# Performance work log

Measured on AMD Instinct MI355X. Metric: run time of the kernel, lower is better.

## Reference

```python
import jax, jax.numpy as jnp
import numpy as np

B, T, I = 16384, 50, 5
H = 128
PRED_LEN = 12


def _uniform(key, shape, bound):
    return jax.random.uniform(key, shape, jnp.float32, -bound, bound)


def setup_inputs() -> dict:
    key = jax.random.key(0)
    ks = jax.random.split(key, 12)
    bound = 1.0 / np.sqrt(H)  # PyTorch LSTM/Linear default init
    return {
        "x": jax.random.normal(ks[0], (B, T, I), jnp.float32),
        "enc_Wih": _uniform(ks[1], (4 * H, I), bound),
        "enc_Whh": _uniform(ks[2], (4 * H, H), bound),
        "enc_bih": _uniform(ks[3], (4 * H,), bound),
        "enc_bhh": _uniform(ks[4], (4 * H,), bound),
        "dec_Wih": _uniform(ks[5], (4 * H, I), bound),
        "dec_Whh": _uniform(ks[6], (4 * H, H), bound),
        "dec_bih": _uniform(ks[7], (4 * H,), bound),
        "dec_bhh": _uniform(ks[8], (4 * H,), bound),
        "lin_W": _uniform(ks[9], (2, H), bound),
        "lin_b": _uniform(ks[10], (2,), bound),
    }


def _lstm_cell(x_t, h, c, Wih, Whh, bih, bhh):
    # PyTorch gate order: i, f, g, o
    gates = x_t @ Wih.T + h @ Whh.T + (bih + bhh)  # [B, 4H]
    i, f, g, o = jnp.split(gates, 4, axis=-1)
    i = jax.nn.sigmoid(i)
    f = jax.nn.sigmoid(f)
    g = jnp.tanh(g)
    o = jax.nn.sigmoid(o)
    c_new = f * c + i * g
    h_new = o * jnp.tanh(c_new)
    return h_new, c_new


def reference(x, enc_Wih, enc_Whh, enc_bih, enc_bhh,
              dec_Wih, dec_Whh, dec_bih, dec_bhh, lin_W, lin_b):
    b = x.shape[0]
    h0 = jnp.zeros((b, H), x.dtype)
    c0 = jnp.zeros((b, H), x.dtype)

    # ---- encoder LSTM over the history sequence ----
    def enc_step(carry, x_t):
        h, c = carry
        h, c = _lstm_cell(x_t, h, c, enc_Wih, enc_Whh, enc_bih, enc_bhh)
        return (h, c), None

    (h, c), _ = jax.lax.scan(enc_step, (h0, c0), jnp.swapaxes(x, 0, 1))

    static_context = x[:, -1, 2:]          # [B, I-2]
    last_velocity = x[:, -1, :2]           # [B, 2]
    dec_in0 = jnp.concatenate([last_velocity, static_context], axis=1)  # [B, I]

    def dec_step(carry, _):
        h, c, dec_in = carry
        h, c = _lstm_cell(dec_in, h, c, dec_Wih, dec_Whh, dec_bih, dec_bhh)
        pred = h @ lin_W.T + lin_b                      # [B, 2]
        dec_in = jnp.concatenate([pred, static_context], axis=1)
        return (h, c, dec_in), pred

    _, preds = jax.lax.scan(dec_step, (h, c, dec_in0), None, length=PRED_LEN)
    return jnp.swapaxes(preds, 0, 1)  # [B, pred_len, 2]
```

## Files before the change

### kernel.cpp

```cpp
#include <hip/hip_runtime.h>
#include <cstdint>

#define TT 50
#define II 5
#define PRED 12

typedef _Float16 f16;
typedef _Float16 f16x8 __attribute__((ext_vector_type(8)));
typedef float f32x4 __attribute__((ext_vector_type(4)));

__global__ void prep_weights(const float* __restrict__ Wih, const float* __restrict__ Whh,
                             const float* __restrict__ bih, const float* __restrict__ bhh,
                             f16* __restrict__ outw) {
    int f = blockIdx.x * 256 + threadIdx.x;
    if (f >= 81920) return;
    int j  = f & 7;
    int c  = (f >> 3) & 15;
    int q  = (f >> 7) & 3;
    int t2 = f >> 9;
    int kc = t2 % 5;
    int wg = t2 / 5;
    int w = wg >> 2, gsub = wg & 3;
    int g = gsub * 128 + w * 16 + c;
    int k = kc * 32 + q * 8 + j;
    float v;
    if (k < 128)       v = Whh[g * 128 + k];
    else if (k < 133)  v = Wih[g * 5 + (k - 128)];
    else if (k == 133) v = bih[g] + bhh[g];
    else               v = 0.f;
    outw[f] = (f16)v;
}

__device__ __forceinline__ float fsig(float x) {
    return __builtin_amdgcn_rcpf(1.f + __builtin_amdgcn_exp2f(-1.4426950408889634f * x));
}
__device__ __forceinline__ float ftanh(float x) {
    return 1.f - 2.f * __builtin_amdgcn_rcpf(1.f + __builtin_amdgcn_exp2f(2.885390081777927f * x));
}

__global__ __launch_bounds__(512, 2)
void lstm_kernel(const float* __restrict__ x,
                 const f16* __restrict__ wfrag,
                 const float* __restrict__ linW, const float* __restrict__ linB,
                 float* __restrict__ out) {
    __shared__ __align__(16) unsigned char state[64 * 512];
    __shared__ float predpart[8][64][2];

    const int tid  = threadIdx.x;
    const int lane = tid & 63;
    const int w    = tid >> 6;
    const int q    = lane >> 4;
    const int cl   = lane & 15;
    const int s0   = blockIdx.x * 64;
    const int jb   = w * 16 + q * 4;
    const int physh = ((jb >> 3) ^ (2 * cl)) & 31;
    const int hoff  = (jb & 7) * 2;

    f16x8 wr[4][5];
    {
        const f16x8* wp = (const f16x8*)wfrag;
        #pragma unroll
        for (int gs = 0; gs < 4; ++gs) {
            #pragma unroll
            for (int kc = 0; kc < 5; ++kc)
                wr[gs][kc] = wp[((w * 4 + gs) * 5 + kc) * 64 + lane];
        }
    }
    float w0r[4], w1r[4];
    #pragma unroll
    for (int idx = 0; idx < 4; ++idx) {
        w0r[idx] = linW[jb + idx];
        w1r[idx] = linW[128 + jb + idx];
    }
    float sc0 = 0.f, sc1 = 0.f, sc2 = 0.f;
    if (tid < 64) {
        const float* xr = x + (size_t)(s0 + tid) * (TT * II) + 49 * II;
        sc0 = xr[2]; sc1 = xr[3]; sc2 = xr[4];
    }
    {
        uint32_t* sp = (uint32_t*)state;
        #pragma unroll
        for (int r = 0; r < 16; ++r) sp[tid + r * 512] = 0u;
    }
    float creg[4][4];
    #pragma unroll
    for (int a = 0; a < 4; ++a)
        #pragma unroll
        for (int b = 0; b < 4; ++b) creg[a][b] = 0.f;

    __syncthreads();
    if (tid < 64) {
        const float* xr = x + (size_t)(s0 + tid) * (TT * II);
        union { f16 h[8]; uint4 u; } pk;
        pk.h[0] = (f16)xr[0]; pk.h[1] = (f16)xr[1]; pk.h[2] = (f16)xr[2];
        pk.h[3] = (f16)xr[3]; pk.h[4] = (f16)xr[4];
        pk.h[5] = (f16)1.f; pk.h[6] = (f16)0.f; pk.h[7] = (f16)0.f;
        int phys = 16 ^ (2 * (tid & 15));
        *(uint4*)(state + tid * 512 + phys * 16) = pk.u;
    }
    __syncthreads();

    f32x4 zero4 = {0.f, 0.f, 0.f, 0.f};

    #pragma unroll 1
    for (int t = 0; t < TT; ++t) {
        float xv0 = 0, xv1 = 0, xv2 = 0, xv3 = 0, xv4 = 0;
        if (tid < 64) {
            int tn = (t < TT - 1) ? t + 1 : TT - 1;
            const float* xr = x + (size_t)(s0 + tid) * (TT * II) + tn * II;
            xv0 = xr[0]; xv1 = xr[1]; xv2 = xr[2]; xv3 = xr[3]; xv4 = xr[4];
        }
        f32x4 acc[4][4];
        #pragma unroll
        for (int gs = 0; gs < 4; ++gs)
            #pragma unroll
            for (int ns = 0; ns < 4; ++ns) acc[gs][ns] = zero4;

        #pragma unroll
        for (int ns = 0; ns < 4; ++ns) {
            const int srow = ns * 16 + cl;
            #pragma unroll
            for (int kc = 0; kc < 5; ++kc) {
                const int phys = (kc * 4 + q) ^ (2 * cl);
                f16x8 bf = *(const f16x8*)(state + srow * 512 + phys * 16);
                acc[0][ns] = __builtin_amdgcn_mfma_f32_16x16x32_f16(wr[0][kc], bf, acc[0][ns], 0, 0, 0);
                acc[1][ns] = __builtin_amdgcn_mfma_f32_16x16x32_f16(wr[1][kc], bf, acc[1][ns], 0, 0, 0);
                acc[2][ns] = __builtin_amdgcn_mfma_f32_16x16x32_f16(wr[2][kc], bf, acc[2][ns], 0, 0, 0);
                acc[3][ns] = __builtin_amdgcn_mfma_f32_16x16x32_f16(wr[3][kc], bf, acc[3][ns], 0, 0, 0);
            }
        }
        uint2 hp[4];
        #pragma unroll
        for (int ns = 0; ns < 4; ++ns) {
            union { f16 h[4]; uint2 u; } pk;
            #pragma unroll
            for (int idx = 0; idx < 4; ++idx) {
                float ii = fsig(acc[0][ns][idx]);
                float ff = fsig(acc[1][ns][idx]);
                float gg = ftanh(acc[2][ns][idx]);
                float oo = fsig(acc[3][ns][idx]);
                float cn = ff * creg[ns][idx] + ii * gg;
                creg[ns][idx] = cn;
                pk.h[idx] = (f16)(oo * ftanh(cn));
            }
            hp[ns] = pk.u;
        }
        __syncthreads();
        #pragma unroll
        for (int ns = 0; ns < 4; ++ns)
            *(uint2*)(state + (ns * 16 + cl) * 512 + physh * 16 + hoff) = hp[ns];
        if (tid < 64) {
            union { f16 h[8]; uint4 u; } pk;
            pk.h[0] = (f16)xv0; pk.h[1] = (f16)xv1; pk.h[2] = (f16)xv2;
            pk.h[3] = (f16)xv3; pk.h[4] = (f16)xv4;
            pk.h[5] = (f16)1.f; pk.h[6] = (f16)0.f; pk.h[7] = (f16)0.f;
            int phys = 16 ^ (2 * (tid & 15));
            *(uint4*)(state + tid * 512 + phys * 16) = pk.u;
        }
        __syncthreads();
    }

    {
        const f16x8* wp = (const f16x8*)(wfrag + 81920);
        #pragma unroll
        for (int gs = 0; gs < 4; ++gs) {
            #pragma unroll
            for (int kc = 0; kc < 5; ++kc)
                wr[gs][kc] = wp[((w * 4 + gs) * 5 + kc) * 64 + lane];
        }
    }

    #pragma unroll 1
    for (int td = 0; td < PRED; ++td) {
        f32x4 acc[4][4];
        #pragma unroll
        for (int gs = 0; gs < 4; ++gs)
            #pragma unroll
            for (int ns = 0; ns < 4; ++ns) acc[gs][ns] = zero4;

        #pragma unroll
        for (int ns = 0; ns < 4; ++ns) {
            const int srow = ns * 16 + cl;
            #pragma unroll
            for (int kc = 0; kc < 5; ++kc) {
                const int phys = (kc * 4 + q) ^ (2 * cl);
                f16x8 bf = *(const f16x8*)(state + srow * 512 + phys * 16);
                acc[0][ns] = __builtin_amdgcn_mfma_f32_16x16x32_f16(wr[0][kc], bf, acc[0][ns], 0, 0, 0);
                acc[1][ns] = __builtin_amdgcn_mfma_f32_16x16x32_f16(wr[1][kc], bf, acc[1][ns], 0, 0, 0);
                acc[2][ns] = __builtin_amdgcn_mfma_f32_16x16x32_f16(wr[2][kc], bf, acc[2][ns], 0, 0, 0);
                acc[3][ns] = __builtin_amdgcn_mfma_f32_16x16x32_f16(wr[3][kc], bf, acc[3][ns], 0, 0, 0);
            }
        }
        uint2 hp[4];
        float p0[4], p1[4];
        #pragma unroll
        for (int ns = 0; ns < 4; ++ns) {
            union { f16 h[4]; uint2 u; } pk;
            p0[ns] = 0.f; p1[ns] = 0.f;
            #pragma unroll
            for (int idx = 0; idx < 4; ++idx) {
                float ii = fsig(acc[0][ns][idx]);
                float ff = fsig(acc[1][ns][idx]);
                float gg = ftanh(acc[2][ns][idx]);
                float oo = fsig(acc[3][ns][idx]);
                float cn = ff * creg[ns][idx] + ii * gg;
                creg[ns][idx] = cn;
                float hv = oo * ftanh(cn);
                p0[ns] += hv * w0r[idx];
                p1[ns] += hv * w1r[idx];
                pk.h[idx] = (f16)hv;
            }
            hp[ns] = pk.u;
        }
        #pragma unroll
        for (int ns = 0; ns < 4; ++ns) {
            p0[ns] += __shfl_xor(p0[ns], 16);
            p0[ns] += __shfl_xor(p0[ns], 32);
            p1[ns] += __shfl_xor(p1[ns], 16);
            p1[ns] += __shfl_xor(p1[ns], 32);
        }
        if (q == 0) {
            #pragma unroll
            for (int ns = 0; ns < 4; ++ns) {
                predpart[w][ns * 16 + cl][0] = p0[ns];
                predpart[w][ns * 16 + cl][1] = p1[ns];
            }
        }
        __syncthreads();
        #pragma unroll
        for (int ns = 0; ns < 4; ++ns)
            *(uint2*)(state + (ns * 16 + cl) * 512 + physh * 16 + hoff) = hp[ns];
        if (tid < 64) {
            float a0 = linB[0], a1 = linB[1];
            #pragma unroll
            for (int ww = 0; ww < 8; ++ww) {
                a0 += predpart[ww][tid][0];
                a1 += predpart[ww][tid][1];
            }
            float2 o2; o2.x = a0; o2.y = a1;
            *(float2*)(out + (size_t)(s0 + tid) * (PRED * 2) + td * 2) = o2;
            union { f16 h[8]; uint4 u; } pk;
            pk.h[0] = (f16)a0; pk.h[1] = (f16)a1;
            pk.h[2] = (f16)sc0; pk.h[3] = (f16)sc1; pk.h[4] = (f16)sc2;
            pk.h[5] = (f16)1.f; pk.h[6] = (f16)0.f; pk.h[7] = (f16)0.f;
            int phys = 16 ^ (2 * (tid & 15));
            *(uint4*)(state + tid * 512 + phys * 16) = pk.u;
        }
        __syncthreads();
    }
}

extern "C" void kernel_launch(void* const* d_in, const int* in_sizes, int n_in,
                              void* d_out, int out_size, void* d_ws, size_t ws_size,
                              hipStream_t stream) {
    (void)in_sizes; (void)n_in; (void)out_size; (void)ws_size;
    const float* x    = (const float*)d_in[0];
    const float* eWih = (const float*)d_in[1];
    const float* eWhh = (const float*)d_in[2];
    const float* ebih = (const float*)d_in[3];
    const float* ebhh = (const float*)d_in[4];
    const float* dWih = (const float*)d_in[5];
    const float* dWhh = (const float*)d_in[6];
    const float* dbih = (const float*)d_in[7];
    const float* dbhh = (const float*)d_in[8];
    const float* linW = (const float*)d_in[9];
    const float* linB = (const float*)d_in[10];
    f16* wfrag = (f16*)d_ws;

    prep_weights<<<320, 256, 0, stream>>>(eWih, eWhh, ebih, ebhh, wfrag);
    prep_weights<<<320, 256, 0, stream>>>(dWih, dWhh, dbih, dbhh, wfrag + 81920);
    lstm_kernel<<<256, 512, 0, stream>>>(x, wfrag, linW, linB, (float*)d_out);
}
```

Before: 281.0 us.

## Split batch tile into two half-groups and overlap MFMA with activations

The 64-sample tile is split into two 32-sample halves (A and B) with double-buffered LDS state. In the encoder, the MFMA for one half is interleaved with the gate activations of the other, so matrix and transcendental work can overlap within each barrier interval. The weight-prep kernels are removed and weights are converted to fp16 fragments directly in registers inside the main kernel. The cell activation is rewritten with fewer reciprocals and a clamped tanh. This adds LDS usage and register pressure, and every block now converts the weights itself, repeating that work across all blocks.

```diff
diff --git a/kernel.cpp b/kernel.cpp
--- a/kernel.cpp
+++ b/kernel.cpp
@@ -9,42 +9,123 @@
 typedef _Float16 f16x8 __attribute__((ext_vector_type(8)));
 typedef float f32x4 __attribute__((ext_vector_type(4)));
 
-__global__ void prep_weights(const float* __restrict__ Wih, const float* __restrict__ Whh,
-                             const float* __restrict__ bih, const float* __restrict__ bhh,
-                             f16* __restrict__ outw) {
-    int f = blockIdx.x * 256 + threadIdx.x;
-    if (f >= 81920) return;
-    int j  = f & 7;
-    int c  = (f >> 3) & 15;
-    int q  = (f >> 7) & 3;
-    int t2 = f >> 9;
-    int kc = t2 % 5;
-    int wg = t2 / 5;
-    int w = wg >> 2, gsub = wg & 3;
-    int g = gsub * 128 + w * 16 + c;
-    int k = kc * 32 + q * 8 + j;
-    float v;
-    if (k < 128)       v = Whh[g * 128 + k];
-    else if (k < 133)  v = Wih[g * 5 + (k - 128)];
-    else if (k == 133) v = bih[g] + bhh[g];
-    else               v = 0.f;
-    outw[f] = (f16)v;
-}
-
-__device__ __forceinline__ float fsig(float x) {
-    return __builtin_amdgcn_rcpf(1.f + __builtin_amdgcn_exp2f(-1.4426950408889634f * x));
-}
-__device__ __forceinline__ float ftanh(float x) {
-    return 1.f - 2.f * __builtin_amdgcn_rcpf(1.f + __builtin_amdgcn_exp2f(2.885390081777927f * x));
+#define K1 1.4426950408889634f
+#define K2 2.8853900817779268f
+
+__device__ __forceinline__ float cellact(float xi, float xf, float xg, float xo, float& c) {
+    float ea = __builtin_amdgcn_exp2f(xi * -K1);
+    float ef = __builtin_amdgcn_exp2f(xf * -K1);
+    float eg = __builtin_amdgcn_exp2f(xg *  K2);
+    float eo = __builtin_amdgcn_exp2f(xo * -K1);
+    float a1 = 1.f + ea, a2 = 1.f + ef, a3 = eg + 1.f, a4 = eg - 1.f;
+    float t1 = a1 * a3;
+    float cn = fmaf(c, t1, a4 * a2) * __builtin_amdgcn_rcpf(t1 * a2);
+    c = cn;
+    float cc = fminf(fmaxf(cn, -15.f), 15.f);
+    float ec = __builtin_amdgcn_exp2f(cc * K2);
+    return (ec - 1.f) * __builtin_amdgcn_rcpf((1.f + eo) * (ec + 1.f));
+}
+
+__device__ __forceinline__ void load_weights(const float* __restrict__ Wih, const float* __restrict__ Whh,
+                                             const float* __restrict__ bih, const float* __restrict__ bhh,
+                                             f16x8 wr[4][5], int w, int cl, int q) {
+    #pragma unroll
+    for (int gs = 0; gs < 4; ++gs) {
+        const int g = gs * 128 + w * 16 + cl;
+        const float* row = Whh + g * 128 + q * 8;
+        #pragma unroll
+        for (int kc = 0; kc < 4; ++kc) {
+            float4 a = *(const float4*)(row + kc * 32);
+            float4 b = *(const float4*)(row + kc * 32 + 4);
+            f16x8 r;
+            r[0] = (f16)a.x; r[1] = (f16)a.y; r[2] = (f16)a.z; r[3] = (f16)a.w;
+            r[4] = (f16)b.x; r[5] = (f16)b.y; r[6] = (f16)b.z; r[7] = (f16)b.w;
+            wr[gs][kc] = r;
+        }
+        f16x8 r;
+        #pragma unroll
+        for (int j = 0; j < 8; ++j) {
+            int k = 128 + q * 8 + j;
+            float v = 0.f;
+            if (k < 133)       v = Wih[g * 5 + (k - 128)];
+            else if (k == 133) v = bih[g] + bhh[g];
+            r[j] = (f16)v;
+        }
+        wr[gs][4] = r;
+    }
+}
+
+__device__ __forceinline__ void do_mfma(const unsigned char* sb, const f16x8 wr[4][5],
+                                        f32x4 acc[4][2], int cl, int q) {
+    #pragma unroll
+    for (int ns = 0; ns < 2; ++ns) {
+        const int srow = ns * 16 + cl;
+        #pragma unroll
+        for (int kc = 0; kc < 5; ++kc) {
+            const int phys = (kc * 4 + q) ^ (2 * cl);
+            f16x8 bf = *(const f16x8*)(sb + srow * 512 + phys * 16);
+            acc[0][ns] = __builtin_amdgcn_mfma_f32_16x16x32_f16(wr[0][kc], bf, acc[0][ns], 0, 0, 0);
+            acc[1][ns] = __builtin_amdgcn_mfma_f32_16x16x32_f16(wr[1][kc], bf, acc[1][ns], 0, 0, 0);
+            acc[2][ns] = __builtin_amdgcn_mfma_f32_16x16x32_f16(wr[2][kc], bf, acc[2][ns], 0, 0, 0);
+            acc[3][ns] = __builtin_amdgcn_mfma_f32_16x16x32_f16(wr[3][kc], bf, acc[3][ns], 0, 0, 0);
+        }
+    }
+}
+
+__device__ __forceinline__ void do_act(f32x4 acc[4][2], float creg[2][4], unsigned char* dst,
+                                       int cl, int physh, int hoff) {
+    #pragma unroll
+    for (int ns = 0; ns < 2; ++ns) {
+        union { f16 h[4]; uint2 u; } pk;
+        #pragma unroll
+        for (int idx = 0; idx < 4; ++idx)
+            pk.h[idx] = (f16)cellact(acc[0][ns][idx], acc[1][ns][idx], acc[2][ns][idx],
+                                     acc[3][ns][idx], creg[ns][idx]);
+        *(uint2*)(dst + (ns * 16 + cl) * 512 + physh * 16 + hoff) = pk.u;
+    }
+}
+
+__device__ __forceinline__ void do_act_dec(f32x4 acc[4][2], float creg[2][4], unsigned char* dst,
+                                           int cl, int physh, int hoff,
+                                           const float w0r[4], const float w1r[4],
+                                           float p0[2], float p1[2]) {
+    #pragma unroll
+    for (int ns = 0; ns < 2; ++ns) {
+        union { f16 h[4]; uint2 u; } pk;
+        p0[ns] = 0.f; p1[ns] = 0.f;
+        #pragma unroll
+        for (int idx = 0; idx < 4; ++idx) {
+            float hv = cellact(acc[0][ns][idx], acc[1][ns][idx], acc[2][ns][idx],
+                               acc[3][ns][idx], creg[ns][idx]);
+            p0[ns] = fmaf(hv, w0r[idx], p0[ns]);
+            p1[ns] = fmaf(hv, w1r[idx], p1[ns]);
+            pk.h[idx] = (f16)hv;
+        }
+        *(uint2*)(dst + (ns * 16 + cl) * 512 + physh * 16 + hoff) = pk.u;
+    }
+}
+
+__device__ __forceinline__ void write_x5(unsigned char* sb, int sl,
+                                         float v0, float v1, float v2, float v3, float v4) {
+    union { f16 h[8]; uint4 u; } pk;
+    pk.h[0] = (f16)v0; pk.h[1] = (f16)v1; pk.h[2] = (f16)v2;
+    pk.h[3] = (f16)v3; pk.h[4] = (f16)v4;
+    pk.h[5] = (f16)1.f; pk.h[6] = (f16)0.f; pk.h[7] = (f16)0.f;
+    int phys = 16 ^ (2 * (sl & 15));
+    *(uint4*)(sb + sl * 512 + phys * 16) = pk.u;
 }
 
 __global__ __launch_bounds__(512, 2)
 void lstm_kernel(const float* __restrict__ x,
-                 const f16* __restrict__ wfrag,
+                 const float* __restrict__ eWih, const float* __restrict__ eWhh,
+                 const float* __restrict__ ebih, const float* __restrict__ ebhh,
+                 const float* __restrict__ dWih, const float* __restrict__ dWhh,
+                 const float* __restrict__ dbih, const float* __restrict__ dbhh,
                  const float* __restrict__ linW, const float* __restrict__ linB,
                  float* __restrict__ out) {
-    __shared__ __align__(16) unsigned char state[64 * 512];
-    __shared__ float predpart[8][64][2];
+    __shared__ __align__(16) unsigned char stateA[2][32 * 512];
+    __shared__ __align__(16) unsigned char stateB[2][32 * 512];
+    __shared__ float ppA[8][32][2], ppB[8][32][2];
 
     const int tid  = threadIdx.x;
     const int lane = tid & 63;
@@ -57,194 +138,114 @@
     const int hoff  = (jb & 7) * 2;
 
     f16x8 wr[4][5];
+    load_weights(eWih, eWhh, ebih, ebhh, wr, w, cl, q);
+
     {
-        const f16x8* wp = (const f16x8*)wfrag;
-        #pragma unroll
-        for (int gs = 0; gs < 4; ++gs) {
-            #pragma unroll
-            for (int kc = 0; kc < 5; ++kc)
-                wr[gs][kc] = wp[((w * 4 + gs) * 5 + kc) * 64 + lane];
-        }
-    }
+        uint4 z{0, 0, 0, 0};
+        uint4* pa = (uint4*)&stateA[0][0];
+        uint4* pb = (uint4*)&stateB[0][0];
+        #pragma unroll
+        for (int r = 0; r < 4; ++r) { pa[tid + r * 512] = z; pb[tid + r * 512] = z; }
+    }
+    float cregA[2][4], cregB[2][4];
+    #pragma unroll
+    for (int a = 0; a < 2; ++a)
+        #pragma unroll
+        for (int b = 0; b < 4; ++b) { cregA[a][b] = 0.f; cregB[a][b] = 0.f; }
+    f32x4 accA[4][2], accB[4][2];
+    const f32x4 z4 = {0.f, 0.f, 0.f, 0.f};
+
+    __syncthreads();
+    if (tid < 32) {
+        const float* xr = x + (size_t)(s0 + tid) * (TT * II);
+        write_x5(stateA[0], tid, xr[0], xr[1], xr[2], xr[3], xr[4]);
+    }
+    __syncthreads();
+
+    #pragma unroll 1
+    for (int t = 0; t < TT; ++t) {
+        unsigned char* curA = stateA[t & 1];
+        unsigned char* nxtA = stateA[(t + 1) & 1];
+        unsigned char* curB = stateB[t & 1];
+        float xv0 = 0, xv1 = 0, xv2 = 0, xv3 = 0, xv4 = 0;
+        if (tid < 64) {
+            int tl = (tid < 32) ? ((t < TT - 1) ? t + 1 : TT - 1) : t;
+            const float* xr = x + (size_t)(s0 + tid) * (TT * II) + tl * II;
+            xv0 = xr[0]; xv1 = xr[1]; xv2 = xr[2]; xv3 = xr[3]; xv4 = xr[4];
+        }
+        #pragma unroll
+        for (int gs = 0; gs < 4; ++gs) { accA[gs][0] = z4; accA[gs][1] = z4; }
+        do_mfma(curA, wr, accA, cl, q);
+        if (t > 0) do_act(accB, cregB, curB, cl, physh, hoff);
+        if (tid >= 32 && tid < 64) write_x5(curB, tid - 32, xv0, xv1, xv2, xv3, xv4);
+        __syncthreads();
+        #pragma unroll
+        for (int gs = 0; gs < 4; ++gs) { accB[gs][0] = z4; accB[gs][1] = z4; }
+        do_mfma(curB, wr, accB, cl, q);
+        do_act(accA, cregA, nxtA, cl, physh, hoff);
+        if (tid < 32) write_x5(nxtA, tid, xv0, xv1, xv2, xv3, xv4);
+        __syncthreads();
+    }
+    do_act(accB, cregB, stateB[0], cl, physh, hoff);
+    if (tid >= 32 && tid < 64) {
+        const float* xr = x + (size_t)(s0 + tid) * (TT * II) + (TT - 1) * II;
+        write_x5(stateB[0], tid - 32, xr[0], xr[1], xr[2], xr[3], xr[4]);
+    }
+    __syncthreads();
+
+    load_weights(dWih, dWhh, dbih, dbhh, wr, w, cl, q);
     float w0r[4], w1r[4];
     #pragma unroll
     for (int idx = 0; idx < 4; ++idx) {
         w0r[idx] = linW[jb + idx];
         w1r[idx] = linW[128 + jb + idx];
     }
-    float sc0 = 0.f, sc1 = 0.f, sc2 = 0.f;
+    float sc0 = 0, sc1 = 0, sc2 = 0, lb0 = 0, lb1 = 0;
     if (tid < 64) {
-        const float* xr = x + (size_t)(s0 + tid) * (TT * II) + 49 * II;
+        const float* xr = x + (size_t)(s0 + tid) * (TT * II) + (TT - 1) * II;
         sc0 = xr[2]; sc1 = xr[3]; sc2 = xr[4];
-    }
-    {
-        uint32_t* sp = (uint32_t*)state;
-        #pragma unroll
-        for (int r = 0; r < 16; ++r) sp[tid + r * 512] = 0u;
-    }
-    float creg[4][4];
-    #pragma unroll
-    for (int a = 0; a < 4; ++a)
-        #pragma unroll
-        for (int b = 0; b < 4; ++b) creg[a][b] = 0.f;
-
-    __syncthreads();
-    if (tid < 64) {
-        const float* xr = x + (size_t)(s0 + tid) * (TT * II);
-        union { f16 h[8]; uint4 u; } pk;
-        pk.h[0] = (f16)xr[0]; pk.h[1] = (f16)xr[1]; pk.h[2] = (f16)xr[2];
-        pk.h[3] = (f16)xr[3]; pk.h[4] = (f16)xr[4];
-        pk.h[5] = (f16)1.f; pk.h[6] = (f16)0.f; pk.h[7] = (f16)0.f;
-        int phys = 16 ^ (2 * (tid & 15));
-        *(uint4*)(state + tid * 512 + phys * 16) = pk.u;
-    }
-    __syncthreads();
-
-    f32x4 zero4 = {0.f, 0.f, 0.f, 0.f};
+        lb0 = linB[0]; lb1 = linB[1];
+    }
 
     #pragma unroll 1
-    for (int t = 0; t < TT; ++t) {
-        float xv0 = 0, xv1 = 0, xv2 = 0, xv3 = 0, xv4 = 0;
-        if (tid < 64) {
-            int tn = (t < TT - 1) ? t + 1 : TT - 1;
-            const float* xr = x + (size_t)(s0 + tid) * (TT * II) + tn * II;
-            xv0 = xr[0]; xv1 = xr[1]; xv2 = xr[2]; xv3 = xr[3]; xv4 = xr[4];
-        }
-        f32x4 acc[4][4];
-        #pragma unroll
-        for (int gs = 0; gs < 4; ++gs)
-            #pragma unroll
-            for (int ns = 0; ns < 4; ++ns) acc[gs][ns] = zero4;
-
-        #pragma unroll
-        for (int ns = 0; ns < 4; ++ns) {
-            const int srow = ns * 16 + cl;
-            #pragma unroll
-            for (int kc = 0; kc < 5; ++kc) {
-                const int phys = (kc * 4 + q) ^ (2 * cl);
-                f16x8 bf = *(const f16x8*)(state + srow * 512 + phys * 16);
-                acc[0][ns] = __builtin_amdgcn_mfma_f32_16x16x32_f16(wr[0][kc], bf, acc[0][ns], 0, 0, 0);
-                acc[1][ns] = __builtin_amdgcn_mfma_f32_16x16x32_f16(wr[1][kc], bf, acc[1][ns], 0, 0, 0);
-                acc[2][ns] = __builtin_amdgcn_mfma_f32_16x16x32_f16(wr[2][kc], bf, acc[2][ns], 0, 0, 0);
-                acc[3][ns] = __builtin_amdgcn_mfma_f32_16x16x32_f16(wr[3][kc], bf, acc[3][ns], 0, 0, 0);
-            }
-        }
-        uint2 hp[4];
-        #pragma unroll
-        for (int ns = 0; ns < 4; ++ns) {
-            union { f16 h[4]; uint2 u; } pk;
-            #pragma unroll
-            for (int idx = 0; idx < 4; ++idx) {
-                float ii = fsig(acc[0][ns][idx]);
-                float ff = fsig(acc[1][ns][idx]);
-                float gg = ftanh(acc[2][ns][idx]);
-                float oo = fsig(acc[3][ns][idx]);
-                float cn = ff * creg[ns][idx] + ii * gg;
-                creg[ns][idx] = cn;
-                pk.h[idx] = (f16)(oo * ftanh(cn));
-            }
-            hp[ns] = pk.u;
-        }
-        __syncthreads();
-        #pragma unroll
-        for (int ns = 0; ns < 4; ++ns)
-            *(uint2*)(state + (ns * 16 + cl) * 512 + physh * 16 + hoff) = hp[ns];
-        if (tid < 64) {
-            union { f16 h[8]; uint4 u; } pk;
-            pk.h[0] = (f16)xv0; pk.h[1] = (f16)xv1; pk.h[2] = (f16)xv2;
-            pk.h[3] = (f16)xv3; pk.h[4] = (f16)xv4;
-            pk.h[5] = (f16)1.f; pk.h[6] = (f16)0.f; pk.h[7] = (f16)0.f;
-            int phys = 16 ^ (2 * (tid & 15));
-            *(uint4*)(state + tid * 512 + phys * 16) = pk.u;
-        }
-        __syncthreads();
-    }
-
-    {
-        const f16x8* wp = (const f16x8*)(wfrag + 81920);
+    for (int dt = 0; dt < PRED; ++dt) {
+        int t = TT + dt;
+        unsigned char* curA = stateA[t & 1]; unsigned char* nxtA = stateA[(t + 1) & 1];
+        unsigned char* curB = stateB[t & 1]; unsigned char* nxtB = stateB[(t + 1) & 1];
         #pragma unroll
         for (int gs = 0; gs < 4; ++gs) {
-            #pragma unroll
-            for (int kc = 0; kc < 5; ++kc)
-                wr[gs][kc] = wp[((w * 4 + gs) * 5 + kc) * 64 + lane];
-        }
-    }
-
-    #pragma unroll 1
-    for (int td = 0; td < PRED; ++td) {
-        f32x4 acc[4][4];
-        #pragma unroll
-        for (int gs = 0; gs < 4; ++gs)
-            #pragma unroll
-            for (int ns = 0; ns < 4; ++ns) acc[gs][ns] = zero4;
-
-        #pragma unroll
-        for (int ns = 0; ns < 4; ++ns) {
-            const int srow = ns * 16 + cl;
-            #pragma unroll
-            for (int kc = 0; kc < 5; ++kc) {
-                const int phys = (kc * 4 + q) ^ (2 * cl);
-                f16x8 bf = *(const f16x8*)(state + srow * 512 + phys * 16);
-                acc[0][ns] = __builtin_amdgcn_mfma_f32_16x16x32_f16(wr[0][kc], bf, acc[0][ns], 0, 0, 0);
-                acc[1][ns] = __builtin_amdgcn_mfma_f32_16x16x32_f16(wr[1][kc], bf, acc[1][ns], 0, 0, 0);
-                acc[2][ns] = __builtin_amdgcn_mfma_f32_16x16x32_f16(wr[2][kc], bf, acc[2][ns], 0, 0, 0);
-                acc[3][ns] = __builtin_amdgcn_mfma_f32_16x16x32_f16(wr[3][kc], bf, acc[3][ns], 0, 0, 0);
-            }
-        }
-        uint2 hp[4];
-        float p0[4], p1[4];
-        #pragma unroll
-        for (int ns = 0; ns < 4; ++ns) {
-            union { f16 h[4]; uint2 u; } pk;
-            p0[ns] = 0.f; p1[ns] = 0.f;
-            #pragma unroll
-            for (int idx = 0; idx < 4; ++idx) {
-                float ii = fsig(acc[0][ns][idx]);
-                float ff = fsig(acc[1][ns][idx]);
-                float gg = ftanh(acc[2][ns][idx]);
-                float oo = fsig(acc[3][ns][idx]);
-                float cn = ff * creg[ns][idx] + ii * gg;
-                creg[ns][idx] = cn;
-                float hv = oo * ftanh(cn);
-                p0[ns] += hv * w0r[idx];
-                p1[ns] += hv * w1r[idx];
-                pk.h[idx] = (f16)hv;
-            }
-            hp[ns] = pk.u;
-        }
-        #pragma unroll
-        for (int ns = 0; ns < 4; ++ns) {
-            p0[ns] += __shfl_xor(p0[ns], 16);
-            p0[ns] += __shfl_xor(p0[ns], 32);
-            p1[ns] += __shfl_xor(p1[ns], 16);
-            p1[ns] += __shfl_xor(p1[ns], 32);
+            accA[gs][0] = z4; accA[gs][1] = z4;
+            accB[gs][0] = z4; accB[gs][1] = z4;
+        }
+        do_mfma(curA, wr, accA, cl, q);
+        do_mfma(curB, wr, accB, cl, q);
+        float p0A[2], p1A[2], p0B[2], p1B[2];
+        do_act_dec(accA, cregA, nxtA, cl, physh, hoff, w0r, w1r, p0A, p1A);
+        do_act_dec(accB, cregB, nxtB, cl, physh, hoff, w0r, w1r, p0B, p1B);
+        #pragma unroll
+        for (int ns = 0; ns < 2; ++ns) {
+            p0A[ns] += __shfl_xor(p0A[ns], 16); p0A[ns] += __shfl_xor(p0A[ns], 32);
+            p1A[ns] += __shfl_xor(p1A[ns], 16); p1A[ns] += __shfl_xor(p1A[ns], 32);
+            p0B[ns] += __shfl_xor(p0B[ns], 16); p0B[ns] += __shfl_xor(p0B[ns], 32);
+            p1B[ns] += __shfl_xor(p1B[ns], 16); p1B[ns] += __shfl_xor(p1B[ns], 32);
         }
         if (q == 0) {
             #pragma unroll
-            for (int ns = 0; ns < 4; ++ns) {
-                predpart[w][ns * 16 + cl][0] = p0[ns];
-                predpart[w][ns * 16 + cl][1] = p1[ns];
+            for (int ns = 0; ns < 2; ++ns) {
+                ppA[w][ns * 16 + cl][0] = p0A[ns]; ppA[w][ns * 16 + cl][1] = p1A[ns];
+                ppB[w][ns * 16 + cl][0] = p0B[ns]; ppB[w][ns * 16 + cl][1] = p1B[ns];
             }
         }
         __syncthreads();
-        #pragma unroll
-        for (int ns = 0; ns < 4; ++ns)
-            *(uint2*)(state + (ns * 16 + cl) * 512 + physh * 16 + hoff) = hp[ns];
         if (tid < 64) {
-            float a0 = linB[0], a1 = linB[1];
+            int sl = tid & 31;
+            float (*pp)[32][2] = (tid < 32) ? ppA : ppB;
+            float a0 = lb0, a1 = lb1;
             #pragma unroll
-            for (int ww = 0; ww < 8; ++ww) {
-                a0 += predpart[ww][tid][0];
-                a1 += predpart[ww][tid][1];
-            }
+            for (int ww = 0; ww < 8; ++ww) { a0 += pp[ww][sl][0]; a1 += pp[ww][sl][1]; }
             float2 o2; o2.x = a0; o2.y = a1;
-            *(float2*)(out + (size_t)(s0 + tid) * (PRED * 2) + td * 2) = o2;
-            union { f16 h[8]; uint4 u; } pk;
-            pk.h[0] = (f16)a0; pk.h[1] = (f16)a1;
-            pk.h[2] = (f16)sc0; pk.h[3] = (f16)sc1; pk.h[4] = (f16)sc2;
-            pk.h[5] = (f16)1.f; pk.h[6] = (f16)0.f; pk.h[7] = (f16)0.f;
-            int phys = 16 ^ (2 * (tid & 15));
-            *(uint4*)(state + tid * 512 + phys * 16) = pk.u;
+            *(float2*)(out + (size_t)(s0 + tid) * (PRED * 2) + dt * 2) = o2;
+            write_x5((tid < 32) ? nxtA : nxtB, sl, a0, a1, sc0, sc1, sc2);
         }
         __syncthreads();
     }
@@ -253,7 +254,7 @@
 extern "C" void kernel_launch(void* const* d_in, const int* in_sizes, int n_in,
                               void* d_out, int out_size, void* d_ws, size_t ws_size,
                               hipStream_t stream) {
-    (void)in_sizes; (void)n_in; (void)out_size; (void)ws_size;
+    (void)in_sizes; (void)n_in; (void)out_size; (void)d_ws; (void)ws_size;
     const float* x    = (const float*)d_in[0];
     const float* eWih = (const float*)d_in[1];
     const float* eWhh = (const float*)d_in[2];
@@ -265,9 +266,8 @@
     const float* dbhh = (const float*)d_in[8];
     const float* linW = (const float*)d_in[9];
     const float* linB = (const float*)d_in[10];
-    f16* wfrag = (f16*)d_ws;
-
-    prep_weights<<<320, 256, 0, stream>>>(eWih, eWhh, ebih, ebhh, wfrag);
-    prep_weights<<<320, 256, 0, stream>>>(dWih, dWhh, dbih, dbhh, wfrag + 81920);
-    lstm_kernel<<<256, 512, 0, stream>>>(x, wfrag, linW, linB, (float*)d_out);
-}
+
+    lstm_kernel<<<256, 512, 0, stream>>>(x, eWih, eWhh, ebih, ebhh,
+                                         dWih, dWhh, dbih, dbhh,
+                                         linW, linB, (float*)d_out);
+}
```

Result: slower. 290.6 us (+3.4%).
